# Performance work log

Measured on AMD Instinct MI355X. Metric: run time of the kernel, lower is better.

The kernel has to match this reference:

```python
import jax, jax.numpy as jnp
import numpy as np

N_NODES = 50000
N_EDGES = 800000
HID = 128
EDGE_FEAT = 4
NUM_G = 20
R_MIN, R_MAX = 0.0, 100.0  # r_max = 10.0**2


def _mlp2(x, w1, b1, w2, b2, act_last):
    y = jax.nn.relu(x @ w1 + b1)
    y = y @ w2 + b2
    return jax.nn.relu(y) if act_last else y


def _linear_init(key, fan_in, fan_out):
    kw, kb = jax.random.split(key)
    lim = 1.0 / np.sqrt(fan_in)
    w = jax.random.uniform(kw, (fan_in, fan_out), jnp.float32, -lim, lim)
    b = jax.random.uniform(kb, (fan_out,), jnp.float32, -lim, lim)
    return w, b


def setup_inputs():
    key = jax.random.key(0)
    ks = jax.random.split(key, 16)
    src = jax.random.randint(ks[0], (N_EDGES,), 0, N_NODES)
    dst = jax.random.randint(ks[1], (N_EDGES,), 0, N_NODES)
    edge_feat = jax.random.normal(ks[2], (N_EDGES, EDGE_FEAT), jnp.float32)
    h = jax.random.normal(ks[3], (N_NODES, HID), jnp.float32)
    x = jax.random.normal(ks[4], (N_NODES, 3), jnp.float32)
    ein = 2 * HID + EDGE_FEAT + NUM_G
    ew1, eb1 = _linear_init(ks[5], ein, HID)
    ew2, eb2 = _linear_init(ks[6], HID, HID)
    infw, infb = _linear_init(ks[7], HID, 1)
    xw1, xb1 = _linear_init(ks[8], HID, HID)
    xw2, xb2 = _linear_init(ks[9], HID, 1)
    nw1, nb1 = _linear_init(ks[10], 2 * HID, HID)
    nw2, nb2 = _linear_init(ks[11], HID, HID)
    return {"src": src, "dst": dst, "edge_feat": edge_feat, "h": h, "x": x,
            "ew1": ew1, "eb1": eb1, "ew2": ew2, "eb2": eb2,
            "infw": infw, "infb": infb,
            "xw1": xw1, "xb1": xb1, "xw2": xw2, "xb2": xb2,
            "nw1": nw1, "nb1": nb1, "nw2": nw2, "nb2": nb2}


def reference(src, dst, edge_feat, h, x,
              ew1, eb1, ew2, eb2, infw, infb,
              xw1, xb1, xw2, xb2, nw1, nb1, nw2, nb2):
    n_nodes = h.shape[0]
    rel_x = x[dst] - x[src]                      # [E, 3]
    r = jnp.sum(rel_x * rel_x, -1, keepdims=True)  # [E, 1]
    # GaussianSmearing expansion
    offsets = jnp.linspace(R_MIN, R_MAX, NUM_G)
    coeff = -0.5 / (offsets[1] - offsets[0]) ** 2
    r_feat = jnp.exp(coeff * (r - offsets) ** 2)  # [E, NUM_G]
    # edge message MLP (act_last=True)
    cat = jnp.concatenate([edge_feat, r_feat, h[dst], h[src]], axis=-1)
    mij = _mlp2(cat, ew1, eb1, ew2, eb2, act_last=True)  # [E, HID]
    eij = jax.nn.sigmoid(mij @ infw + infb)              # [E, 1]
    mi = jax.ops.segment_sum(mij * eij, dst, num_segments=n_nodes)  # [N, HID]
    h_new = h + _mlp2(jnp.concatenate([mi, h], -1), nw1, nb1, nw2, nb2, act_last=False)
    # coordinate update: (xi - xj) == rel_x
    x_scale = _mlp2(mij, xw1, xb1, xw2, xb2, act_last=False)  # [E, 1]
    delta_x = jax.ops.segment_sum(rel_x * x_scale, dst, num_segments=n_nodes)
    x_new = x + delta_x
    return h_new, x_new
```

## Files before the change

kernel.cpp:

```cpp
#include <hip/hip_runtime.h>

#define HID 128
#define NNODES 50000
#define NEDGES 800000

typedef __attribute__((ext_vector_type(8))) short short8;
typedef __attribute__((ext_vector_type(4))) float f32x4;

union U8 { short8 v; unsigned short u[8]; };

__device__ __forceinline__ unsigned short f2b(float f) {
  unsigned int u = __float_as_uint(f);
  u += 0x7FFFu + ((u >> 16) & 1u);
  return (unsigned short)(u >> 16);
}

__device__ __forceinline__ unsigned int pk2(float a, float b) {
  unsigned int ua = __float_as_uint(a);
  ua += 0x7FFFu + ((ua >> 16) & 1u);
  unsigned int ub = __float_as_uint(b);
  ub += 0x7FFFu + ((ub >> 16) & 1u);
  return (ua >> 16) | (ub & 0xFFFF0000u);
}

__device__ __forceinline__ void atomicPkAddBf16(unsigned short* addr, unsigned int packed) {
  asm volatile("global_atomic_pk_add_bf16 %0, %1, off" :: "v"(addr), "v"(packed) : "memory");
}

__global__ __launch_bounds__(256) void pack_kernel(
    const float* __restrict__ ew1, const float* __restrict__ ew2,
    const float* __restrict__ xw1, const float* __restrict__ nw1,
    const float* __restrict__ nw2, unsigned short* __restrict__ ws) {
  int i = blockIdx.x * 256 + threadIdx.x;
  const float* w; int base, ksrc;
  if (i < 36864)       { w = ew1; base = 0;      ksrc = 280; }
  else if (i < 53248)  { w = ew2; base = 36864;  ksrc = 128; }
  else if (i < 69632)  { w = xw1; base = 53248;  ksrc = 128; }
  else if (i < 102400) { w = nw1; base = 69632;  ksrc = 256; }
  else if (i < 118784) { w = nw2; base = 102400; ksrc = 128; }
  else return;
  int li = i - base;
  int j = li & 7, t = li >> 3;
  int col = t & 127, kg = t >> 7;
  int k = kg * 8 + j;
  float v = (k < ksrc) ? w[k * 128 + col] : 0.0f;
  ws[i] = f2b(v);
}

__global__ __launch_bounds__(256) void hpack_kernel(
    const float* __restrict__ h, unsigned short* __restrict__ hB) {
  int i = blockIdx.x * 256 + threadIdx.x;
  const float4* p = reinterpret_cast<const float4*>(h + (size_t)i * 8);
  float4 a = p[0], b = p[1];
  uint4 u;
  u.x = pk2(a.x, a.y); u.y = pk2(a.z, a.w);
  u.z = pk2(b.x, b.y); u.w = pk2(b.z, b.w);
  *reinterpret_cast<uint4*>(hB + (size_t)i * 8) = u;
}

template<int MODE>
__global__ __launch_bounds__(256, 4) void edge_kernel(
    const int* __restrict__ src, const int* __restrict__ dst,
    const float* __restrict__ ef, const float* __restrict__ h,
    const float* __restrict__ x,
    const float* __restrict__ eb1, const float* __restrict__ eb2,
    const float* __restrict__ infw, const float* __restrict__ infb,
    const float* __restrict__ xb1, const float* __restrict__ xw2,
    const float* __restrict__ xb2,
    const short8* __restrict__ W1p, const short8* __restrict__ W2p,
    const short8* __restrict__ XW1p,
    const unsigned short* __restrict__ hB,
    float* __restrict__ miF, unsigned short* __restrict__ miB,
    float* __restrict__ dx) {
  __shared__ __align__(16) char catB[64 * 576];
  __shared__ int dL[64], sL[64];
  __shared__ float relL[64][3];
  __shared__ float ppart[4][64];
  __shared__ float eijL[64];

  const int tid = threadIdx.x;
  const int e0 = blockIdx.x * 64;
  const int lane = tid & 63, w = tid >> 6;
  const int lr = lane & 15, lg = lane >> 4;
  const int l7 = lr & 7, l3 = lr & 3;
  const int colb = w*32 + lr;

  {
    int row = tid >> 2, sub = tid & 3;
    int e = e0 + row;
    int s = src[e], d = dst[e];
    if (sub == 0) { sL[row] = s; dL[row] = d; }
    float rx = x[3*d+0] - x[3*s+0];
    float ry = x[3*d+1] - x[3*s+1];
    float rz = x[3*d+2] - x[3*s+2];
    if (sub == 1) { relL[row][0] = rx; relL[row][1] = ry; relL[row][2] = rz; }
    float r = rx*rx + ry*ry + rz*rz;
    const float step = 100.0f / 19.0f;
    const float co = -0.5f / (step * step);
    float v6[6];
    if (sub == 0) {
      const float4 efv = reinterpret_cast<const float4*>(ef)[e];
      v6[0]=efv.x; v6[1]=efv.y; v6[2]=efv.z; v6[3]=efv.w;
      float t1 = r - step;
      v6[4] = __expf(co * r * r);
      v6[5] = __expf(co * t1 * t1);
    } else {
      #pragma unroll
      for (int q = 0; q < 6; ++q) {
        float g = (float)(sub*6 - 4 + q) * step;
        float t = r - g;
        v6[q] = __expf(co * t * t);
      }
    }
    #pragma unroll
    for (int q = 0; q < 3; ++q) {
      int c = sub*6 + q*2;
      int chunk = (c>>3) ^ (row&7);
      *reinterpret_cast<unsigned int*>(catB + row*576 + (chunk<<4) + ((c&7)<<1)) = pk2(v6[q*2], v6[q*2+1]);
    }
    if (sub == 3) {
      U8 z;
      #pragma unroll
      for (int j = 0; j < 8; ++j) z.u[j] = 0;
      *reinterpret_cast<short8*>(catB + row*576 + ((32 + (3 ^ (row&3)))<<4)) = z.v;
    }
  }

  #pragma unroll
  for (int it = 0; it < 8; ++it) {
    int i = tid + it*256;
    int row = i >> 5, c = i & 31;
    int node = (c < 16) ? dst[e0+row] : src[e0+row];
    int chunk = 3 + c;
    int sw = (chunk < 32) ? (chunk ^ (row&7)) : (32 + ((chunk&3) ^ (row&3)));
    if (MODE == 2) {
      short8 u = *reinterpret_cast<const short8*>(hB + (size_t)node*128 + (c&15)*8);
      *reinterpret_cast<short8*>(catB + row*576 + (sw<<4)) = u;
    } else {
      const float4* hp = reinterpret_cast<const float4*>(h + (size_t)node*128 + (c&15)*8);
      float4 a = hp[0], b = hp[1];
      uint4 u;
      u.x = pk2(a.x, a.y); u.y = pk2(a.z, a.w);
      u.z = pk2(b.x, b.y); u.w = pk2(b.z, b.w);
      *reinterpret_cast<uint4*>(catB + row*576 + (sw<<4)) = u;
    }
  }

  short8 p00 = W1p[(0*4+lg)*128 + colb], p01 = W1p[(0*4+lg)*128 + colb + 16];
  short8 p10 = W1p[(1*4+lg)*128 + colb], p11 = W1p[(1*4+lg)*128 + colb + 16];
  __syncthreads();

  f32x4 acc[4][2];
  #pragma unroll
  for (int t = 0; t < 4; ++t) { acc[t][0] = (f32x4)0.0f; acc[t][1] = (f32x4)0.0f; }
  #pragma unroll
  for (int kt = 0; kt < 9; ++kt) {
    int ch = (kt < 8) ? ((kt*4+lg) ^ l7) : (32 + (lg ^ l3));
    short8 a0 = *reinterpret_cast<const short8*>(catB + (0*16+lr)*576 + (ch<<4));
    short8 a1 = *reinterpret_cast<const short8*>(catB + (1*16+lr)*576 + (ch<<4));
    short8 a2 = *reinterpret_cast<const short8*>(catB + (2*16+lr)*576 + (ch<<4));
    short8 a3 = *reinterpret_cast<const short8*>(catB + (3*16+lr)*576 + (ch<<4));
    short8 b0, b1;
    if (kt == 0)      { b0 = p00; b1 = p01; }
    else if (kt == 1) { b0 = p10; b1 = p11; }
    else              { b0 = W1p[(kt*4+lg)*128 + colb]; b1 = W1p[(kt*4+lg)*128 + colb + 16]; }
    acc[0][0] = __builtin_amdgcn_mfma_f32_16x16x32_bf16(a0, b0, acc[0][0], 0, 0, 0);
    acc[0][1] = __builtin_amdgcn_mfma_f32_16x16x32_bf16(a0, b1, acc[0][1], 0, 0, 0);
    acc[1][0] = __builtin_amdgcn_mfma_f32_16x16x32_bf16(a1, b0, acc[1][0], 0, 0, 0);
    acc[1][1] = __builtin_amdgcn_mfma_f32_16x16x32_bf16(a1, b1, acc[1][1], 0, 0, 0);
    acc[2][0] = __builtin_amdgcn_mfma_f32_16x16x32_bf16(a2, b0, acc[2][0], 0, 0, 0);
    acc[2][1] = __builtin_amdgcn_mfma_f32_16x16x32_bf16(a2, b1, acc[2][1], 0, 0, 0);
    acc[3][0] = __builtin_amdgcn_mfma_f32_16x16x32_bf16(a3, b0, acc[3][0], 0, 0, 0);
    acc[3][1] = __builtin_amdgcn_mfma_f32_16x16x32_bf16(a3, b1, acc[3][1], 0, 0, 0);
  }
  __syncthreads();

  {
    float be0 = eb1[colb], be1 = eb1[colb+16];
    #pragma unroll
    for (int t = 0; t < 4; ++t)
      #pragma unroll
      for (int rg = 0; rg < 4; ++rg) {
        int row = t*16 + lg*4 + rg;
        float v0 = fmaxf(acc[t][0][rg] + be0, 0.f);
        float v1 = fmaxf(acc[t][1][rg] + be1, 0.f);
        float send = (lr & 1) ? v0 : v1;
        float got = __shfl_xor(send, 1, 64);
        int col0; unsigned int pv;
        if (!(lr & 1)) { col0 = w*32 + lr;          pv = pk2(v0, got); }
        else           { col0 = w*32 + 16 + lr - 1; pv = pk2(got, v1); }
        int chunk = (col0>>3) ^ (row&7);
        *reinterpret_cast<unsigned int*>(catB + row*576 + (chunk<<4) + ((col0&7)<<1)) = pv;
      }
  }
  __syncthreads();

  f32x4 acc2[4][2];
  #pragma unroll
  for (int t = 0; t < 4; ++t) { acc2[t][0] = (f32x4)0.0f; acc2[t][1] = (f32x4)0.0f; }
  #pragma unroll
  for (int kt = 0; kt < 4; ++kt) {
    int ch = (kt*4+lg) ^ l7;
    short8 a0 = *reinterpret_cast<const short8*>(catB + (0*16+lr)*576 + (ch<<4));
    short8 a1 = *reinterpret_cast<const short8*>(catB + (1*16+lr)*576 + (ch<<4));
    short8 a2 = *reinterpret_cast<const short8*>(catB + (2*16+lr)*576 + (ch<<4));
    short8 a3 = *reinterpret_cast<const short8*>(catB + (3*16+lr)*576 + (ch<<4));
    short8 b0 = W2p[(kt*4+lg)*128 + colb];
    short8 b1 = W2p[(kt*4+lg)*128 + colb + 16];
    acc2[0][0] = __builtin_amdgcn_mfma_f32_16x16x32_bf16(a0, b0, acc2[0][0], 0, 0, 0);
    acc2[0][1] = __builtin_amdgcn_mfma_f32_16x16x32_bf16(a0, b1, acc2[0][1], 0, 0, 0);
    acc2[1][0] = __builtin_amdgcn_mfma_f32_16x16x32_bf16(a1, b0, acc2[1][0], 0, 0, 0);
    acc2[1][1] = __builtin_amdgcn_mfma_f32_16x16x32_bf16(a1, b1, acc2[1][1], 0, 0, 0);
    acc2[2][0] = __builtin_amdgcn_mfma_f32_16x16x32_bf16(a2, b0, acc2[2][0], 0, 0, 0);
    acc2[2][1] = __builtin_amdgcn_mfma_f32_16x16x32_bf16(a2, b1, acc2[2][1], 0, 0, 0);
    acc2[3][0] = __builtin_amdgcn_mfma_f32_16x16x32_bf16(a3, b0, acc2[3][0], 0, 0, 0);
    acc2[3][1] = __builtin_amdgcn_mfma_f32_16x16x32_bf16(a3, b1, acc2[3][1], 0, 0, 0);
  }
  {
    float be0 = eb2[colb], be1 = eb2[colb+16];
    float iw0 = infw[colb], iw1 = infw[colb+16];
    float pl[4][4];
    #pragma unroll
    for (int t = 0; t < 4; ++t)
      #pragma unroll
      for (int rg = 0; rg < 4; ++rg) pl[t][rg] = 0.f;
    #pragma unroll
    for (int t = 0; t < 4; ++t)
      #pragma unroll
      for (int rg = 0; rg < 4; ++rg) {
        int row = t*16 + lg*4 + rg;
        float v0 = fmaxf(acc2[t][0][rg] + be0, 0.f);
        float v1 = fmaxf(acc2[t][1][rg] + be1, 0.f);
        acc2[t][0][rg] = v0; acc2[t][1][rg] = v1;
        pl[t][rg] += v0*iw0 + v1*iw1;
        float send = (lr & 1) ? v0 : v1;
        float got = __shfl_xor(send, 1, 64);
        int col0; unsigned int pv;
        if (!(lr & 1)) { col0 = w*32 + lr;          pv = pk2(v0, got); }
        else           { col0 = w*32 + 16 + lr - 1; pv = pk2(got, v1); }
        int chunk = 16 + (((col0>>3)&15) ^ (row&7));
        *reinterpret_cast<unsigned int*>(catB + row*576 + (chunk<<4) + ((col0&7)<<1)) = pv;
      }
    #pragma unroll
    for (int m = 1; m < 16; m <<= 1)
      #pragma unroll
      for (int t = 0; t < 4; ++t)
        #pragma unroll
        for (int rg = 0; rg < 4; ++rg) pl[t][rg] += __shfl_xor(pl[t][rg], m, 64);
    if (lr == 0) {
      #pragma unroll
      for (int t = 0; t < 4; ++t)
        #pragma unroll
        for (int rg = 0; rg < 4; ++rg) ppart[w][t*16 + lg*4 + rg] = pl[t][rg];
    }
  }
  __syncthreads();

  if (lane < 16) {
    int row2 = w*16 + lane;
    float s2 = ppart[0][row2] + ppart[1][row2] + ppart[2][row2] + ppart[3][row2] + infb[0];
    eijL[row2] = 1.f / (1.f + __expf(-s2));
  }
  __syncthreads();

  #pragma unroll
  for (int t = 0; t < 4; ++t)
    #pragma unroll
    for (int rg = 0; rg < 4; ++rg) {
      int row = t*16 + lg*4 + rg;
      int d = dL[row];
      float e = eijL[row];
      float u0 = acc2[t][0][rg] * e;
      float u1 = acc2[t][1][rg] * e;
      if (MODE >= 1) {
        float got = __shfl_xor((lr & 1) ? u0 : u1, 1, 64);
        int col0; unsigned int packed;
        if (!(lr & 1)) { col0 = w*32 + lr;          packed = pk2(u0, got); }
        else           { col0 = w*32 + 16 + lr - 1; packed = pk2(got, u1); }
        atomicPkAddBf16(miB + (size_t)d*128 + col0, packed);
      } else {
        atomicAdd(miF + (size_t)d*128 + colb,      u0);
        atomicAdd(miF + (size_t)d*128 + colb + 16, u1);
      }
    }

  f32x4 acc3[4][2];
  #pragma unroll
  for (int t = 0; t < 4; ++t) { acc3[t][0] = (f32x4)0.0f; acc3[t][1] = (f32x4)0.0f; }
  #pragma unroll
  for (int kt = 0; kt < 4; ++kt) {
    int ch = 16 + ((kt*4+lg) ^ l7);
    short8 a0 = *reinterpret_cast<const short8*>(catB + (0*16+lr)*576 + (ch<<4));
    short8 a1 = *reinterpret_cast<const short8*>(catB + (1*16+lr)*576 + (ch<<4));
    short8 a2 = *reinterpret_cast<const short8*>(catB + (2*16+lr)*576 + (ch<<4));
    short8 a3 = *reinterpret_cast<const short8*>(catB + (3*16+lr)*576 + (ch<<4));
    short8 b0 = XW1p[(kt*4+lg)*128 + colb];
    short8 b1 = XW1p[(kt*4+lg)*128 + colb + 16];
    acc3[0][0] = __builtin_amdgcn_mfma_f32_16x16x32_bf16(a0, b0, acc3[0][0], 0, 0, 0);
    acc3[0][1] = __builtin_amdgcn_mfma_f32_16x16x32_bf16(a0, b1, acc3[0][1], 0, 0, 0);
    acc3[1][0] = __builtin_amdgcn_mfma_f32_16x16x32_bf16(a1, b0, acc3[1][0], 0, 0, 0);
    acc3[1][1] = __builtin_amdgcn_mfma_f32_16x16x32_bf16(a1, b1, acc3[1][1], 0, 0, 0);
    acc3[2][0] = __builtin_amdgcn_mfma_f32_16x16x32_bf16(a2, b0, acc3[2][0], 0, 0, 0);
    acc3[2][1] = __builtin_amdgcn_mfma_f32_16x16x32_bf16(a2, b1, acc3[2][1], 0, 0, 0);
    acc3[3][0] = __builtin_amdgcn_mfma_f32_16x16x32_bf16(a3, b0, acc3[3][0], 0, 0, 0);
    acc3[3][1] = __builtin_amdgcn_mfma_f32_16x16x32_bf16(a3, b1, acc3[3][1], 0, 0, 0);
  }
  {
    float bx0 = xb1[colb], bx1 = xb1[colb+16];
    float xwv0 = xw2[colb], xwv1 = xw2[colb+16];
    float ql[4][4];
    #pragma unroll
    for (int t = 0; t < 4; ++t)
      #pragma unroll
      for (int rg = 0; rg < 4; ++rg) ql[t][rg] = 0.f;
    #pragma unroll
    for (int t = 0; t < 4; ++t)
      #pragma unroll
      for (int rg = 0; rg < 4; ++rg) {
        float v0 = fmaxf(acc3[t][0][rg] + bx0, 0.f);
        float v1 = fmaxf(acc3[t][1][rg] + bx1, 0.f);
        ql[t][rg] += v0*xwv0 + v1*xwv1;
      }
    #pragma unroll
    for (int m = 1; m < 16; m <<= 1)
      #pragma unroll
      for (int t = 0; t < 4; ++t)
        #pragma unroll
        for (int rg = 0; rg < 4; ++rg) ql[t][rg] += __shfl_xor(ql[t][rg], m, 64);
    if (lr == 0) {
      #pragma unroll
      for (int t = 0; t < 4; ++t)
        #pragma unroll
        for (int rg = 0; rg < 4; ++rg) ppart[w][t*16 + lg*4 + rg] = ql[t][rg];
    }
  }
  __syncthreads();

  if (tid < 192) {
    int row = tid / 3, c = tid - row*3;
    float q = ppart[0][row] + ppart[1][row] + ppart[2][row] + ppart[3][row] + xb2[0];
    atomicAdd(dx + dL[row]*3 + c, relL[row][c] * q);
  }
}

template<int MODE>
__global__ __launch_bounds__(256) void node_kernel(
    const float* __restrict__ h, const float* __restrict__ x,
    const float* __restrict__ nb1, const float* __restrict__ nb2,
    const short8* __restrict__ NW1p, const short8* __restrict__ NW2p,
    const unsigned short* __restrict__ miB,
    const unsigned short* __restrict__ hB,
    float* __restrict__ out) {
  __shared__ __align__(16) char c2B[64 * 512];
  __shared__ __align__(16) char y3B[64 * 256];
  const int tid = threadIdx.x;
  const int n0 = blockIdx.x * 64;
  const float* mi = out;

  for (int i = tid; i < 64*32; i += 256) {
    int row = i >> 5, c = i & 31;
    int node = n0 + row;
    U8 u;
    if (node < NNODES) {
      if (c < 16 && MODE >= 1) {
        u.v = *reinterpret_cast<const short8*>(miB + (size_t)node*128 + c*8);
      } else if (c >= 16 && MODE == 2) {
        u.v = *reinterpret_cast<const short8*>(hB + (size_t)node*128 + (c-16)*8);
      } else {
        const float4* p = (c < 16)
          ? reinterpret_cast<const float4*>(mi + (size_t)node*128 + c*8)
          : reinterpret_cast<const float4*>(h + (size_t)node*128 + (c-16)*8);
        float4 a = p[0], b = p[1];
        uint4 uu;
        uu.x = pk2(a.x, a.y); uu.y = pk2(a.z, a.w);
        uu.z = pk2(b.x, b.y); uu.w = pk2(b.z, b.w);
        u.v = *reinterpret_cast<short8*>(&uu);
      }
    } else {
      #pragma unroll
      for (int j = 0; j < 8; ++j) u.u[j] = 0;
    }
    *reinterpret_cast<short8*>(c2B + row*512 + ((c ^ (row&7))<<4)) = u.v;
  }
  __syncthreads();

  const int lane = tid & 63, wave = tid >> 6;
  const int lr = lane & 15, lg = lane >> 4;
  const int rb = wave * 16;
  const int arow = rb + lr;

  f32x4 acc[8];
  #pragma unroll
  for (int nt = 0; nt < 8; ++nt) acc[nt] = (f32x4)0.0f;
  #pragma unroll
  for (int kt = 0; kt < 8; ++kt) {
    int chunk = kt*4 + lg;
    short8 a = *reinterpret_cast<const short8*>(c2B + arow*512 + ((chunk ^ (arow&7))<<4));
    const short8* bp = NW1p + chunk*128 + lr;
    #pragma unroll
    for (int nt = 0; nt < 8; ++nt)
      acc[nt] = __builtin_amdgcn_mfma_f32_16x16x32_bf16(a, bp[nt*16], acc[nt], 0, 0, 0);
  }
  #pragma unroll
  for (int nt = 0; nt < 8; ++nt) {
    int col = nt*16 + lr;
    float bias = nb1[col];
    #pragma unroll
    for (int r = 0; r < 4; ++r) {
      int row = rb + lg*4 + r;
      float v = fmaxf(acc[nt][r] + bias, 0.f);
      *reinterpret_cast<unsigned short*>(y3B + row*256 + (((col>>3) ^ (row&7))<<4) + ((col&7)<<1)) = f2b(v);
    }
  }

  f32x4 acc2[8];
  #pragma unroll
  for (int nt = 0; nt < 8; ++nt) acc2[nt] = (f32x4)0.0f;
  #pragma unroll
  for (int kt = 0; kt < 4; ++kt) {
    int chunk = kt*4 + lg;
    short8 a = *reinterpret_cast<const short8*>(y3B + arow*256 + ((chunk ^ (arow&7))<<4));
    const short8* bp = NW2p + chunk*128 + lr;
    #pragma unroll
    for (int nt = 0; nt < 8; ++nt)
      acc2[nt] = __builtin_amdgcn_mfma_f32_16x16x32_bf16(a, bp[nt*16], acc2[nt], 0, 0, 0);
  }
  __syncthreads();
  #pragma unroll
  for (int nt = 0; nt < 8; ++nt) {
    int col = nt*16 + lr;
    float b2 = nb2[col];
    #pragma unroll
    for (int r = 0; r < 4; ++r) {
      int row = rb + lg*4 + r;
      int node = n0 + row;
      if (node < NNODES) {
        int idx = node*128 + col;
        out[idx] = acc2[nt][r] + b2 + h[idx];
      }
    }
  }

  if (tid < 192) {
    int node = n0 + tid/3;
    if (node < NNODES) {
      int idx = node*3 + (tid%3);
      float* xo = out + NNODES*HID;
      xo[idx] = x[idx] + xo[idx];
    }
  }
}

extern "C" void kernel_launch(void* const* d_in, const int* in_sizes, int n_in,
                              void* d_out, int out_size, void* d_ws, size_t ws_size,
                              hipStream_t stream) {
  const int*   src  = (const int*)  d_in[0];
  const int*   dst  = (const int*)  d_in[1];
  const float* ef   = (const float*)d_in[2];
  const float* h    = (const float*)d_in[3];
  const float* x    = (const float*)d_in[4];
  const float* ew1  = (const float*)d_in[5];
  const float* eb1  = (const float*)d_in[6];
  const float* ew2  = (const float*)d_in[7];
  const float* eb2  = (const float*)d_in[8];
  const float* infw = (const float*)d_in[9];
  const float* infb = (const float*)d_in[10];
  const float* xw1  = (const float*)d_in[11];
  const float* xb1  = (const float*)d_in[12];
  const float* xw2  = (const float*)d_in[13];
  const float* xb2  = (const float*)d_in[14];
  const float* nw1  = (const float*)d_in[15];
  const float* nb1  = (const float*)d_in[16];
  const float* nw2  = (const float*)d_in[17];
  const float* nb2  = (const float*)d_in[18];

  float* out = (float*)d_out;
  float* miF = out;
  float* dxp = out + NNODES*HID;
  unsigned short* wsp = (unsigned short*)d_ws;
  unsigned short* miB = wsp + 118784;
  unsigned short* hBp = miB + (size_t)NNODES*HID;

  const size_t MIN = (size_t)NNODES*HID;
  size_t need1 = (118784u + MIN) * 2u;
  size_t need2 = (118784u + 2u*MIN) * 2u;
  int mode = (ws_size >= need2) ? 2 : (ws_size >= need1 ? 1 : 0);

  if (mode >= 1) {
    hipMemsetAsync(miB, 0, MIN*2, stream);
    hipMemsetAsync(dxp, 0, (size_t)NNODES*3*4, stream);
  } else {
    hipMemsetAsync(d_out, 0, (size_t)out_size * sizeof(float), stream);
  }

  pack_kernel<<<464, 256, 0, stream>>>(ew1, ew2, xw1, nw1, nw2, wsp);
  if (mode == 2) hpack_kernel<<<(NNODES*HID)/(256*8), 256, 0, stream>>>(h, hBp);

  if (mode == 2) {
    edge_kernel<2><<<NEDGES/64, 256, 0, stream>>>(
        src, dst, ef, h, x, eb1, eb2, infw, infb, xb1, xw2, xb2,
        (const short8*)wsp, (const short8*)(wsp + 36864), (const short8*)(wsp + 53248),
        hBp, miF, miB, dxp);
    node_kernel<2><<<(NNODES + 63)/64, 256, 0, stream>>>(
        h, x, nb1, nb2,
        (const short8*)(wsp + 69632), (const short8*)(wsp + 102400), miB, hBp, out);
  } else if (mode == 1) {
    edge_kernel<1><<<NEDGES/64, 256, 0, stream>>>(
        src, dst, ef, h, x, eb1, eb2, infw, infb, xb1, xw2, xb2,
        (const short8*)wsp, (const short8*)(wsp + 36864), (const short8*)(wsp + 53248),
        hBp, miF, miB, dxp);
    node_kernel<1><<<(NNODES + 63)/64, 256, 0, stream>>>(
        h, x, nb1, nb2,
        (const short8*)(wsp + 69632), (const short8*)(wsp + 102400), miB, hBp, out);
  } else {
    edge_kernel<0><<<NEDGES/64, 256, 0, stream>>>(
        src, dst, ef, h, x, eb1, eb2, infw, infb, xb1, xw2, xb2,
        (const short8*)wsp, (const short8*)(wsp + 36864), (const short8*)(wsp + 53248),
        hBp, miF, miB, dxp);
    node_kernel<0><<<(NNODES + 63)/64, 256, 0, stream>>>(
        h, x, nb1, nb2,
        (const short8*)(wsp + 69632), (const short8*)(wsp + 102400), miB, hBp, out);
  }
}
```

Baseline: 361.9 us.

## Swap MFMA operands so each lane owns row-contiguous output columns

Result: slower. 814.1 us (+125.0%).

```diff
diff --git a/kernel.cpp b/kernel.cpp
--- a/kernel.cpp
+++ b/kernel.cpp
@@ -20,6 +20,12 @@
   ua += 0x7FFFu + ((ua >> 16) & 1u);
   unsigned int ub = __float_as_uint(b);
   ub += 0x7FFFu + ((ub >> 16) & 1u);
+  return (ua >> 16) | (ub & 0xFFFF0000u);
+}
+
+__device__ __forceinline__ unsigned int pk2h(float a, float b) {
+  unsigned int ua = __float_as_uint(a) + 0x8000u;
+  unsigned int ub = __float_as_uint(b) + 0x8000u;
   return (ua >> 16) | (ub & 0xFFFF0000u);
 }
 
@@ -116,7 +122,7 @@
     for (int q = 0; q < 3; ++q) {
       int c = sub*6 + q*2;
       int chunk = (c>>3) ^ (row&7);
-      *reinterpret_cast<unsigned int*>(catB + row*576 + (chunk<<4) + ((c&7)<<1)) = pk2(v6[q*2], v6[q*2+1]);
+      *reinterpret_cast<unsigned int*>(catB + row*576 + (chunk<<4) + ((c&7)<<1)) = pk2h(v6[q*2], v6[q*2+1]);
     }
     if (sub == 3) {
       U8 z;
@@ -164,34 +170,38 @@
     if (kt == 0)      { b0 = p00; b1 = p01; }
     else if (kt == 1) { b0 = p10; b1 = p11; }
     else              { b0 = W1p[(kt*4+lg)*128 + colb]; b1 = W1p[(kt*4+lg)*128 + colb + 16]; }
-    acc[0][0] = __builtin_amdgcn_mfma_f32_16x16x32_bf16(a0, b0, acc[0][0], 0, 0, 0);
-    acc[0][1] = __builtin_amdgcn_mfma_f32_16x16x32_bf16(a0, b1, acc[0][1], 0, 0, 0);
-    acc[1][0] = __builtin_amdgcn_mfma_f32_16x16x32_bf16(a1, b0, acc[1][0], 0, 0, 0);
-    acc[1][1] = __builtin_amdgcn_mfma_f32_16x16x32_bf16(a1, b1, acc[1][1], 0, 0, 0);
-    acc[2][0] = __builtin_amdgcn_mfma_f32_16x16x32_bf16(a2, b0, acc[2][0], 0, 0, 0);
-    acc[2][1] = __builtin_amdgcn_mfma_f32_16x16x32_bf16(a2, b1, acc[2][1], 0, 0, 0);
-    acc[3][0] = __builtin_amdgcn_mfma_f32_16x16x32_bf16(a3, b0, acc[3][0], 0, 0, 0);
-    acc[3][1] = __builtin_amdgcn_mfma_f32_16x16x32_bf16(a3, b1, acc[3][1], 0, 0, 0);
+    acc[0][0] = __builtin_amdgcn_mfma_f32_16x16x32_bf16(b0, a0, acc[0][0], 0, 0, 0);
+    acc[0][1] = __builtin_amdgcn_mfma_f32_16x16x32_bf16(b1, a0, acc[0][1], 0, 0, 0);
+    acc[1][0] = __builtin_amdgcn_mfma_f32_16x16x32_bf16(b0, a1, acc[1][0], 0, 0, 0);
+    acc[1][1] = __builtin_amdgcn_mfma_f32_16x16x32_bf16(b1, a1, acc[1][1], 0, 0, 0);
+    acc[2][0] = __builtin_amdgcn_mfma_f32_16x16x32_bf16(b0, a2, acc[2][0], 0, 0, 0);
+    acc[2][1] = __builtin_amdgcn_mfma_f32_16x16x32_bf16(b1, a2, acc[2][1], 0, 0, 0);
+    acc[3][0] = __builtin_amdgcn_mfma_f32_16x16x32_bf16(b0, a3, acc[3][0], 0, 0, 0);
+    acc[3][1] = __builtin_amdgcn_mfma_f32_16x16x32_bf16(b1, a3, acc[3][1], 0, 0, 0);
   }
   __syncthreads();
 
   {
-    float be0 = eb1[colb], be1 = eb1[colb+16];
-    #pragma unroll
-    for (int t = 0; t < 4; ++t)
-      #pragma unroll
-      for (int rg = 0; rg < 4; ++rg) {
-        int row = t*16 + lg*4 + rg;
-        float v0 = fmaxf(acc[t][0][rg] + be0, 0.f);
-        float v1 = fmaxf(acc[t][1][rg] + be1, 0.f);
-        float send = (lr & 1) ? v0 : v1;
-        float got = __shfl_xor(send, 1, 64);
-        int col0; unsigned int pv;
-        if (!(lr & 1)) { col0 = w*32 + lr;          pv = pk2(v0, got); }
-        else           { col0 = w*32 + 16 + lr - 1; pv = pk2(got, v1); }
-        int chunk = (col0>>3) ^ (row&7);
-        *reinterpret_cast<unsigned int*>(catB + row*576 + (chunk<<4) + ((col0&7)<<1)) = pv;
-      }
+    const int c00 = w*32 + lg*4, c01 = c00 + 16;
+    float4 be0 = *reinterpret_cast<const float4*>(eb1 + c00);
+    float4 be1 = *reinterpret_cast<const float4*>(eb1 + c01);
+    #pragma unroll
+    for (int t = 0; t < 4; ++t) {
+      int row = t*16 + lr;
+      char* rowB = catB + row*576;
+      #pragma unroll
+      for (int j = 0; j < 2; ++j) {
+        const float4 be = j ? be1 : be0;
+        int c0 = j ? c01 : c00;
+        float v0 = fmaxf(acc[t][j][0] + be.x, 0.f);
+        float v1 = fmaxf(acc[t][j][1] + be.y, 0.f);
+        float v2 = fmaxf(acc[t][j][2] + be.z, 0.f);
+        float v3 = fmaxf(acc[t][j][3] + be.w, 0.f);
+        uint2 pv; pv.x = pk2h(v0, v1); pv.y = pk2h(v2, v3);
+        int chunk = (c0>>3) ^ (row&7);
+        *reinterpret_cast<uint2*>(rowB + (chunk<<4) + ((c0&7)<<1)) = pv;
+      }
+    }
   }
   __syncthreads();
 
@@ -207,51 +217,51 @@
     short8 a3 = *reinterpret_cast<const short8*>(catB + (3*16+lr)*576 + (ch<<4));
     short8 b0 = W2p[(kt*4+lg)*128 + colb];
     short8 b1 = W2p[(kt*4+lg)*128 + colb + 16];
-    acc2[0][0] = __builtin_amdgcn_mfma_f32_16x16x32_bf16(a0, b0, acc2[0][0], 0, 0, 0);
-    acc2[0][1] = __builtin_amdgcn_mfma_f32_16x16x32_bf16(a0, b1, acc2[0][1], 0, 0, 0);
-    acc2[1][0] = __builtin_amdgcn_mfma_f32_16x16x32_bf16(a1, b0, acc2[1][0], 0, 0, 0);
-    acc2[1][1] = __builtin_amdgcn_mfma_f32_16x16x32_bf16(a1, b1, acc2[1][1], 0, 0, 0);
-    acc2[2][0] = __builtin_amdgcn_mfma_f32_16x16x32_bf16(a2, b0, acc2[2][0], 0, 0, 0);
-    acc2[2][1] = __builtin_amdgcn_mfma_f32_16x16x32_bf16(a2, b1, acc2[2][1], 0, 0, 0);
-    acc2[3][0] = __builtin_amdgcn_mfma_f32_16x16x32_bf16(a3, b0, acc2[3][0], 0, 0, 0);
-    acc2[3][1] = __builtin_amdgcn_mfma_f32_16x16x32_bf16(a3, b1, acc2[3][1], 0, 0, 0);
-  }
+    acc2[0][0] = __builtin_amdgcn_mfma_f32_16x16x32_bf16(b0, a0, acc2[0][0], 0, 0, 0);
+    acc2[0][1] = __builtin_amdgcn_mfma_f32_16x16x32_bf16(b1, a0, acc2[0][1], 0, 0, 0);
+    acc2[1][0] = __builtin_amdgcn_mfma_f32_16x16x32_bf16(b0, a1, acc2[1][0], 0, 0, 0);
+    acc2[1][1] = __builtin_amdgcn_mfma_f32_16x16x32_bf16(b1, a1, acc2[1][1], 0, 0, 0);
+    acc2[2][0] = __builtin_amdgcn_mfma_f32_16x16x32_bf16(b0, a2, acc2[2][0], 0, 0, 0);
+    acc2[2][1] = __builtin_amdgcn_mfma_f32_16x16x32_bf16(b1, a2, acc2[2][1], 0, 0, 0);
+    acc2[3][0] = __builtin_amdgcn_mfma_f32_16x16x32_bf16(b0, a3, acc2[3][0], 0, 0, 0);
+    acc2[3][1] = __builtin_amdgcn_mfma_f32_16x16x32_bf16(b1, a3, acc2[3][1], 0, 0, 0);
+  }
+  float pl[4];
   {
-    float be0 = eb2[colb], be1 = eb2[colb+16];
-    float iw0 = infw[colb], iw1 = infw[colb+16];
-    float pl[4][4];
-    #pragma unroll
-    for (int t = 0; t < 4; ++t)
-      #pragma unroll
-      for (int rg = 0; rg < 4; ++rg) pl[t][rg] = 0.f;
-    #pragma unroll
-    for (int t = 0; t < 4; ++t)
-      #pragma unroll
-      for (int rg = 0; rg < 4; ++rg) {
-        int row = t*16 + lg*4 + rg;
-        float v0 = fmaxf(acc2[t][0][rg] + be0, 0.f);
-        float v1 = fmaxf(acc2[t][1][rg] + be1, 0.f);
-        acc2[t][0][rg] = v0; acc2[t][1][rg] = v1;
-        pl[t][rg] += v0*iw0 + v1*iw1;
-        float send = (lr & 1) ? v0 : v1;
-        float got = __shfl_xor(send, 1, 64);
-        int col0; unsigned int pv;
-        if (!(lr & 1)) { col0 = w*32 + lr;          pv = pk2(v0, got); }
-        else           { col0 = w*32 + 16 + lr - 1; pv = pk2(got, v1); }
-        int chunk = 16 + (((col0>>3)&15) ^ (row&7));
-        *reinterpret_cast<unsigned int*>(catB + row*576 + (chunk<<4) + ((col0&7)<<1)) = pv;
-      }
-    #pragma unroll
-    for (int m = 1; m < 16; m <<= 1)
-      #pragma unroll
-      for (int t = 0; t < 4; ++t)
-        #pragma unroll
-        for (int rg = 0; rg < 4; ++rg) pl[t][rg] += __shfl_xor(pl[t][rg], m, 64);
-    if (lr == 0) {
-      #pragma unroll
-      for (int t = 0; t < 4; ++t)
-        #pragma unroll
-        for (int rg = 0; rg < 4; ++rg) ppart[w][t*16 + lg*4 + rg] = pl[t][rg];
+    const int c00 = w*32 + lg*4, c01 = c00 + 16;
+    float4 be0 = *reinterpret_cast<const float4*>(eb2 + c00);
+    float4 be1 = *reinterpret_cast<const float4*>(eb2 + c01);
+    float4 iw0 = *reinterpret_cast<const float4*>(infw + c00);
+    float4 iw1 = *reinterpret_cast<const float4*>(infw + c01);
+    #pragma unroll
+    for (int t = 0; t < 4; ++t) {
+      int row = t*16 + lr;
+      char* rowB = catB + row*576;
+      pl[t] = 0.f;
+      #pragma unroll
+      for (int j = 0; j < 2; ++j) {
+        const float4 be = j ? be1 : be0;
+        const float4 iw = j ? iw1 : iw0;
+        int c0 = j ? c01 : c00;
+        float v0 = fmaxf(acc2[t][j][0] + be.x, 0.f);
+        float v1 = fmaxf(acc2[t][j][1] + be.y, 0.f);
+        float v2 = fmaxf(acc2[t][j][2] + be.z, 0.f);
+        float v3 = fmaxf(acc2[t][j][3] + be.w, 0.f);
+        acc2[t][j][0] = v0; acc2[t][j][1] = v1; acc2[t][j][2] = v2; acc2[t][j][3] = v3;
+        pl[t] += v0*iw.x + v1*iw.y + v2*iw.z + v3*iw.w;
+        uint2 pv; pv.x = pk2h(v0, v1); pv.y = pk2h(v2, v3);
+        int chunk = 16 + ((c0>>3) ^ (row&7));
+        *reinterpret_cast<uint2*>(rowB + (chunk<<4) + ((c0&7)<<1)) = pv;
+      }
+    }
+    #pragma unroll
+    for (int t = 0; t < 4; ++t) {
+      pl[t] += __shfl_xor(pl[t], 16, 64);
+      pl[t] += __shfl_xor(pl[t], 32, 64);
+    }
+    if (lane < 16) {
+      #pragma unroll
+      for (int t = 0; t < 4; ++t) ppart[w][t*16 + lane] = pl[t];
     }
   }
   __syncthreads();
@@ -263,26 +273,32 @@
   }
   __syncthreads();
 
-  #pragma unroll
-  for (int t = 0; t < 4; ++t)
-    #pragma unroll
-    for (int rg = 0; rg < 4; ++rg) {
-      int row = t*16 + lg*4 + rg;
+  {
+    const int c00 = w*32 + lg*4, c01 = c00 + 16;
+    #pragma unroll
+    for (int t = 0; t < 4; ++t) {
+      int row = t*16 + lr;
       int d = dL[row];
       float e = eijL[row];
-      float u0 = acc2[t][0][rg] * e;
-      float u1 = acc2[t][1][rg] * e;
       if (MODE >= 1) {
-        float got = __shfl_xor((lr & 1) ? u0 : u1, 1, 64);
-        int col0; unsigned int packed;
-        if (!(lr & 1)) { col0 = w*32 + lr;          packed = pk2(u0, got); }
-        else           { col0 = w*32 + 16 + lr - 1; packed = pk2(got, u1); }
-        atomicPkAddBf16(miB + (size_t)d*128 + col0, packed);
+        unsigned short* bp = miB + (size_t)d*128;
+        #pragma unroll
+        for (int j = 0; j < 2; ++j) {
+          int c0 = j ? c01 : c00;
+          atomicPkAddBf16(bp + c0,     pk2h(acc2[t][j][0]*e, acc2[t][j][1]*e));
+          atomicPkAddBf16(bp + c0 + 2, pk2h(acc2[t][j][2]*e, acc2[t][j][3]*e));
+        }
       } else {
-        atomicAdd(miF + (size_t)d*128 + colb,      u0);
-        atomicAdd(miF + (size_t)d*128 + colb + 16, u1);
-      }
-    }
+        float* fp = miF + (size_t)d*128;
+        #pragma unroll
+        for (int j = 0; j < 2; ++j) {
+          int c0 = j ? c01 : c00;
+          #pragma unroll
+          for (int rg = 0; rg < 4; ++rg) atomicAdd(fp + c0 + rg, acc2[t][j][rg]*e);
+        }
+      }
+    }
+  }
 
   f32x4 acc3[4][2];
   #pragma unroll
@@ -296,42 +312,40 @@
     short8 a3 = *reinterpret_cast<const short8*>(catB + (3*16+lr)*576 + (ch<<4));
     short8 b0 = XW1p[(kt*4+lg)*128 + colb];
     short8 b1 = XW1p[(kt*4+lg)*128 + colb + 16];
-    acc3[0][0] = __builtin_amdgcn_mfma_f32_16x16x32_bf16(a0, b0, acc3[0][0], 0, 0, 0);
-    acc3[0][1] = __builtin_amdgcn_mfma_f32_16x16x32_bf16(a0, b1, acc3[0][1], 0, 0, 0);
-    acc3[1][0] = __builtin_amdgcn_mfma_f32_16x16x32_bf16(a1, b0, acc3[1][0], 0, 0, 0);
-    acc3[1][1] = __builtin_amdgcn_mfma_f32_16x16x32_bf16(a1, b1, acc3[1][1], 0, 0, 0);
-    acc3[2][0] = __builtin_amdgcn_mfma_f32_16x16x32_bf16(a2, b0, acc3[2][0], 0, 0, 0);
-    acc3[2][1] = __builtin_amdgcn_mfma_f32_16x16x32_bf16(a2, b1, acc3[2][1], 0, 0, 0);
-    acc3[3][0] = __builtin_amdgcn_mfma_f32_16x16x32_bf16(a3, b0, acc3[3][0], 0, 0, 0);
-    acc3[3][1] = __builtin_amdgcn_mfma_f32_16x16x32_bf16(a3, b1, acc3[3][1], 0, 0, 0);
+    acc3[0][0] = __builtin_amdgcn_mfma_f32_16x16x32_bf16(b0, a0, acc3[0][0], 0, 0, 0);
+    acc3[0][1] = __builtin_amdgcn_mfma_f32_16x16x32_bf16(b1, a0, acc3[0][1], 0, 0, 0);
+    acc3[1][0] = __builtin_amdgcn_mfma_f32_16x16x32_bf16(b0, a1, acc3[1][0], 0, 0, 0);
+    acc3[1][1] = __builtin_amdgcn_mfma_f32_16x16x32_bf16(b1, a1, acc3[1][1], 0, 0, 0);
+    acc3[2][0] = __builtin_amdgcn_mfma_f32_16x16x32_bf16(b0, a2, acc3[2][0], 0, 0, 0);
+    acc3[2][1] = __builtin_amdgcn_mfma_f32_16x16x32_bf16(b1, a2, acc3[2][1], 0, 0, 0);
+    acc3[3][0] = __builtin_amdgcn_mfma_f32_16x16x32_bf16(b0, a3, acc3[3][0], 0, 0, 0);
+    acc3[3][1] = __builtin_amdgcn_mfma_f32_16x16x32_bf16(b1, a3, acc3[3][1], 0, 0, 0);
   }
   {
-    float bx0 = xb1[colb], bx1 = xb1[colb+16];
-    float xwv0 = xw2[colb], xwv1 = xw2[colb+16];
-    float ql[4][4];
-    #pragma unroll
-    for (int t = 0; t < 4; ++t)
-      #pragma unroll
-      for (int rg = 0; rg < 4; ++rg) ql[t][rg] = 0.f;
-    #pragma unroll
-    for (int t = 0; t < 4; ++t)
-      #pragma unroll
-      for (int rg = 0; rg < 4; ++rg) {
-        float v0 = fmaxf(acc3[t][0][rg] + bx0, 0.f);
-        float v1 = fmaxf(acc3[t][1][rg] + bx1, 0.f);
-        ql[t][rg] += v0*xwv0 + v1*xwv1;
-      }
-    #pragma unroll
-    for (int m = 1; m < 16; m <<= 1)
-      #pragma unroll
-      for (int t = 0; t < 4; ++t)
-        #pragma unroll
-        for (int rg = 0; rg < 4; ++rg) ql[t][rg] += __shfl_xor(ql[t][rg], m, 64);
-    if (lr == 0) {
-      #pragma unroll
-      for (int t = 0; t < 4; ++t)
-        #pragma unroll
-        for (int rg = 0; rg < 4; ++rg) ppart[w][t*16 + lg*4 + rg] = ql[t][rg];
+    const int c00 = w*32 + lg*4, c01 = c00 + 16;
+    float4 bx0 = *reinterpret_cast<const float4*>(xb1 + c00);
+    float4 bx1 = *reinterpret_cast<const float4*>(xb1 + c01);
+    float4 xw0 = *reinterpret_cast<const float4*>(xw2 + c00);
+    float4 xw1v = *reinterpret_cast<const float4*>(xw2 + c01);
+    float ql[4];
+    #pragma unroll
+    for (int t = 0; t < 4; ++t) {
+      ql[t] = 0.f;
+      #pragma unroll
+      for (int j = 0; j < 2; ++j) {
+        const float4 bx = j ? bx1 : bx0;
+        const float4 xw = j ? xw1v : xw0;
+        ql[t] += fmaxf(acc3[t][j][0] + bx.x, 0.f) * xw.x
+               + fmaxf(acc3[t][j][1] + bx.y, 0.f) * xw.y
+               + fmaxf(acc3[t][j][2] + bx.z, 0.f) * xw.z
+               + fmaxf(acc3[t][j][3] + bx.w, 0.f) * xw.w;
+      }
+      ql[t] += __shfl_xor(ql[t], 16, 64);
+      ql[t] += __shfl_xor(ql[t], 32, 64);
+    }
+    if (lane < 16) {
+      #pragma unroll
+      for (int t = 0; t < 4; ++t) ppart[w][t*16 + lane] = ql[t];
     }
   }
   __syncthreads();
```
